# Kernel tuning notes

Measured on AMD Instinct MI355X. Metric: run time of the kernel, lower is better.

The kernel has to match this reference:

```python
import jax, jax.numpy as jnp
import numpy as np

N, D, L = 8192, 256, 3
DEGREE_P = 0.0078  # ~64 avg degree


def _normalize_adj(g):
    # symmetric normalization with self-loops: D^-1/2 (A + I) D^-1/2
    n = g.shape[0]
    a = g + jnp.eye(n, dtype=g.dtype)
    deg = jnp.sum(a, axis=1)
    dinv = jnp.where(deg > 0, jax.lax.rsqrt(deg), 0.0)
    return a * dinv[:, None] * dinv[None, :]


def _gcn(gn, h, W, b):
    # GCN layer (eval mode, dropout p=0): aggregate -> linear -> relu
    h = gn @ h                      # [N, D] adjacency aggregation
    return jax.nn.relu(h @ W.T + b)  # [N, D]


def setup_inputs() -> dict:
    key = jax.random.key(0)
    ks = jax.random.split(key, 8)
    # sparse binary symmetric adjacency stored dense
    g = (jax.random.uniform(ks[0], (N, N)) < DEGREE_P).astype(jnp.float32)
    g = jnp.maximum(g, g.T)
    h = jax.random.normal(ks[1], (N, D), dtype=jnp.float32)
    s = 1.0 / np.sqrt(D)
    W_down = jax.random.normal(ks[2], (L, D, D), dtype=jnp.float32) * s
    b_down = jnp.zeros((L, D), dtype=jnp.float32)
    W_bottom = jax.random.normal(ks[3], (D, D), dtype=jnp.float32) * s
    b_bottom = jnp.zeros((D,), dtype=jnp.float32)
    W_up = jax.random.normal(ks[4], (L, D, D), dtype=jnp.float32) * s
    b_up = jnp.zeros((L, D), dtype=jnp.float32)
    return dict(g=g, h=h, W_down=W_down, b_down=b_down,
                W_bottom=W_bottom, b_bottom=b_bottom,
                W_up=W_up, b_up=b_up)


def reference(g, h, W_down, b_down, W_bottom, b_bottom, W_up, b_up):
    gn = _normalize_adj(g)
    l_n = W_down.shape[0]
    org_h = h
    down_outs = []
    for i in range(l_n):
        h = _gcn(gn, h, W_down[i], b_down[i])
        down_outs.append(h)
    h = _gcn(gn, h, W_bottom, b_bottom)
    hs = []
    for i in range(l_n):
        h = h + down_outs[l_n - i - 1]   # skip connection
        h = _gcn(gn, h, W_up[i], b_up[i])
        hs.append(h)
    hs.append(h + org_h)
    return jnp.stack(hs)  # [l_n+1, N, D]
```

## Files before the change

### kernel.cpp

```cpp
#include <hip/hip_runtime.h>
#include <cstdint>
#include <cstddef>


#define GN 8192
#define GD 256
#define CAP 320

typedef unsigned int uint32;
using frag_ab = __attribute__((ext_vector_type(8))) short;
using frag_cd = __attribute__((ext_vector_type(4))) float;
using f32x4   = __attribute__((ext_vector_type(4))) float;
using u32x2   = __attribute__((ext_vector_type(2))) uint32;

static __device__ inline unsigned short f2bf(float x) {
    uint32 u = __float_as_uint(x);
    u += 0x7fffu + ((u >> 16) & 1u);
    return (unsigned short)(u >> 16);
}

__global__ __launch_bounds__(256) void k_build(const float* __restrict__ g,
                                               unsigned short* __restrict__ col,
                                               int* __restrict__ cnt,
                                               float* __restrict__ dinv)
{
    __shared__ int s_cnt;
    const int i = blockIdx.x;
    const int tid = threadIdx.x;
    if (tid == 0) s_cnt = 0;
    __syncthreads();
    const f32x4* grow = (const f32x4*)(g + (size_t)i * GN);
    unsigned short* crow = col + (size_t)i * CAP;
    for (int j4 = tid; j4 < GN / 4; j4 += 256) {
        f32x4 v = __builtin_nontemporal_load(grow + j4);
        int j = j4 * 4;
        if (v[0] != 0.0f) { int p = atomicAdd(&s_cnt, 1); if (p < CAP) __builtin_nontemporal_store((unsigned short)(j + 0), crow + p); }
        if (v[1] != 0.0f) { int p = atomicAdd(&s_cnt, 1); if (p < CAP) __builtin_nontemporal_store((unsigned short)(j + 1), crow + p); }
        if (v[2] != 0.0f) { int p = atomicAdd(&s_cnt, 1); if (p < CAP) __builtin_nontemporal_store((unsigned short)(j + 2), crow + p); }
        if (v[3] != 0.0f) { int p = atomicAdd(&s_cnt, 1); if (p < CAP) __builtin_nontemporal_store((unsigned short)(j + 3), crow + p); }
    }
    __syncthreads();
    if (tid == 0) {
        int n = s_cnt; if (n > CAP) n = CAP;
        cnt[i] = n;
        dinv[i] = rsqrtf((float)s_cnt + 1.0f);
    }
}

__global__ __launch_bounds__(256) void k_scale(const float* __restrict__ h,
                                               const float* __restrict__ dinv,
                                               unsigned short* __restrict__ hs_bf)
{
    int idx = blockIdx.x * 256 + threadIdx.x;
    float4 v = ((const float4*)h)[idx];
    int row = idx / (GD / 4);
    float dv = dinv[row];
    ushort4 r;
    r.x = f2bf(v.x * dv); r.y = f2bf(v.y * dv);
    r.z = f2bf(v.z * dv); r.w = f2bf(v.w * dv);
    ((ushort4*)hs_bf)[idx] = r;
}

__global__ __launch_bounds__(256) void k_f2bf(const float* __restrict__ src,
                                              unsigned short* __restrict__ dst)
{
    int idx = blockIdx.x * 256 + threadIdx.x;
    float4 v = ((const float4*)src)[idx];
    ushort4 r;
    r.x = f2bf(v.x); r.y = f2bf(v.y); r.z = f2bf(v.z); r.w = f2bf(v.w);
    ((ushort4*)dst)[idx] = r;
}

__global__ __launch_bounds__(256) void k_spmm(const u32x2* __restrict__ hsw,
                                              const unsigned short* __restrict__ col,
                                              const int* __restrict__ cnt,
                                              const float* __restrict__ dinv,
                                              u32x2* __restrict__ yw)
{
    __shared__ unsigned short s_cols[4][CAP];
    const int tid  = threadIdx.x;
    const int lr   = tid >> 6;
    const int lane = tid & 63;
    const int i    = blockIdx.x * 4 + lr;
    const int n    = cnt[i];
    unsigned short* sc = s_cols[lr];
    const unsigned short* crow = col + (size_t)i * CAP;
    for (int t = lane; t < n; t += 64)
        sc[t] = __builtin_nontemporal_load(crow + t);

    float e0a = 0.f, e1a = 0.f, e2a = 0.f, e3a = 0.f;
    float e0b = 0.f, e1b = 0.f, e2b = 0.f, e3b = 0.f;
    int t = 0;
    for (; t + 8 <= n; t += 8) {
        ushort4 ca = *(const ushort4*)(sc + t);
        ushort4 cb = *(const ushort4*)(sc + t + 4);
        u32x2 u0 = hsw[(uint32)ca.x * 64u + lane];
        u32x2 u1 = hsw[(uint32)ca.y * 64u + lane];
        u32x2 u2 = hsw[(uint32)ca.z * 64u + lane];
        u32x2 u3 = hsw[(uint32)ca.w * 64u + lane];
        u32x2 u4 = hsw[(uint32)cb.x * 64u + lane];
        u32x2 u5 = hsw[(uint32)cb.y * 64u + lane];
        u32x2 u6 = hsw[(uint32)cb.z * 64u + lane];
        u32x2 u7 = hsw[(uint32)cb.w * 64u + lane];
        e0a += __uint_as_float(u0[0] << 16); e1a += __uint_as_float(u0[0] & 0xffff0000u);
        e2a += __uint_as_float(u0[1] << 16); e3a += __uint_as_float(u0[1] & 0xffff0000u);
        e0b += __uint_as_float(u1[0] << 16); e1b += __uint_as_float(u1[0] & 0xffff0000u);
        e2b += __uint_as_float(u1[1] << 16); e3b += __uint_as_float(u1[1] & 0xffff0000u);
        e0a += __uint_as_float(u2[0] << 16); e1a += __uint_as_float(u2[0] & 0xffff0000u);
        e2a += __uint_as_float(u2[1] << 16); e3a += __uint_as_float(u2[1] & 0xffff0000u);
        e0b += __uint_as_float(u3[0] << 16); e1b += __uint_as_float(u3[0] & 0xffff0000u);
        e2b += __uint_as_float(u3[1] << 16); e3b += __uint_as_float(u3[1] & 0xffff0000u);
        e0a += __uint_as_float(u4[0] << 16); e1a += __uint_as_float(u4[0] & 0xffff0000u);
        e2a += __uint_as_float(u4[1] << 16); e3a += __uint_as_float(u4[1] & 0xffff0000u);
        e0b += __uint_as_float(u5[0] << 16); e1b += __uint_as_float(u5[0] & 0xffff0000u);
        e2b += __uint_as_float(u5[1] << 16); e3b += __uint_as_float(u5[1] & 0xffff0000u);
        e0a += __uint_as_float(u6[0] << 16); e1a += __uint_as_float(u6[0] & 0xffff0000u);
        e2a += __uint_as_float(u6[1] << 16); e3a += __uint_as_float(u6[1] & 0xffff0000u);
        e0b += __uint_as_float(u7[0] << 16); e1b += __uint_as_float(u7[0] & 0xffff0000u);
        e2b += __uint_as_float(u7[1] << 16); e3b += __uint_as_float(u7[1] & 0xffff0000u);
    }
    for (; t < n; ++t) {
        u32x2 u = hsw[(uint32)sc[t] * 64u + lane];
        e0a += __uint_as_float(u[0] << 16); e1a += __uint_as_float(u[0] & 0xffff0000u);
        e2a += __uint_as_float(u[1] << 16); e3a += __uint_as_float(u[1] & 0xffff0000u);
    }
    u32x2 us = hsw[(uint32)i * 64u + lane];
    e0b += __uint_as_float(us[0] << 16); e1b += __uint_as_float(us[0] & 0xffff0000u);
    e2b += __uint_as_float(us[1] << 16); e3b += __uint_as_float(us[1] & 0xffff0000u);

    const float dv = dinv[i];
    const float e0 = (e0a + e0b) * dv;
    const float e1 = (e1a + e1b) * dv;
    const float e2 = (e2a + e2b) * dv;
    const float e3 = (e3a + e3b) * dv;
    u32x2 r;
    r[0] = (uint32)f2bf(e0) | ((uint32)f2bf(e1) << 16);
    r[1] = (uint32)f2bf(e2) | ((uint32)f2bf(e3) << 16);
    __builtin_nontemporal_store(r, yw + (uint32)i * 64u + lane);
}

__global__ __launch_bounds__(256) void k_gemm(const unsigned short* __restrict__ Y,
                                              const unsigned short* __restrict__ W,
                                              const float* __restrict__ bias,
                                              const float* __restrict__ dinv,
                                              const float* __restrict__ skip,
                                              float* __restrict__ h_out,
                                              unsigned short* __restrict__ hs_out,
                                              float* __restrict__ sum_out,
                                              const float* __restrict__ add_src)
{
    const int tid  = threadIdx.x;
    const int w    = tid >> 6;
    const int lane = tid & 63;
    const int quad = lane >> 4;
    const int l16  = lane & 15;
    const int m0 = blockIdx.x * 64 + w * 16;
    const int n0 = blockIdx.y * 64;

    frag_cd acc0 = {0.f,0.f,0.f,0.f}, acc1 = {0.f,0.f,0.f,0.f};
    frag_cd acc2 = {0.f,0.f,0.f,0.f}, acc3 = {0.f,0.f,0.f,0.f};

    const size_t abase  = (size_t)(m0 + l16) * GD + quad * 8;
    const size_t bbase0 = (size_t)(n0 +  0 + l16) * GD + quad * 8;
    const size_t bbase1 = (size_t)(n0 + 16 + l16) * GD + quad * 8;
    const size_t bbase2 = (size_t)(n0 + 32 + l16) * GD + quad * 8;
    const size_t bbase3 = (size_t)(n0 + 48 + l16) * GD + quad * 8;

#pragma unroll
    for (int k0 = 0; k0 < GD; k0 += 32) {
        frag_ab a  = *(const frag_ab*)(Y + abase  + k0);
        frag_ab b0 = *(const frag_ab*)(W + bbase0 + k0);
        frag_ab b1 = *(const frag_ab*)(W + bbase1 + k0);
        frag_ab b2 = *(const frag_ab*)(W + bbase2 + k0);
        frag_ab b3 = *(const frag_ab*)(W + bbase3 + k0);
        acc0 = __builtin_amdgcn_mfma_f32_16x16x32_bf16(a, b0, acc0, 0, 0, 0);
        acc1 = __builtin_amdgcn_mfma_f32_16x16x32_bf16(a, b1, acc1, 0, 0, 0);
        acc2 = __builtin_amdgcn_mfma_f32_16x16x32_bf16(a, b2, acc2, 0, 0, 0);
        acc3 = __builtin_amdgcn_mfma_f32_16x16x32_bf16(a, b3, acc3, 0, 0, 0);
    }

    const float bn0 = bias[n0 +  0 + l16];
    const float bn1 = bias[n0 + 16 + l16];
    const float bn2 = bias[n0 + 32 + l16];
    const float bn3 = bias[n0 + 48 + l16];

#pragma unroll
    for (int reg = 0; reg < 4; ++reg) {
        const int m = m0 + quad * 4 + reg;
        const float dv = dinv[m];
        float v[4];
        v[0] = fmaxf(acc0[reg] + bn0, 0.f);
        v[1] = fmaxf(acc1[reg] + bn1, 0.f);
        v[2] = fmaxf(acc2[reg] + bn2, 0.f);
        v[3] = fmaxf(acc3[reg] + bn3, 0.f);
#pragma unroll
        for (int nt = 0; nt < 4; ++nt) {
            const size_t idx = (size_t)m * GD + n0 + nt * 16 + l16;
            const float x = v[nt];
            if (h_out)  __builtin_nontemporal_store(x, h_out + idx);
            if (hs_out) {
                float s = skip ? __builtin_nontemporal_load(skip + idx) : 0.f;
                hs_out[idx] = f2bf(dv * (x + s));
            }
            if (sum_out) __builtin_nontemporal_store(x + __builtin_nontemporal_load(add_src + idx), sum_out + idx);
        }
    }
}

extern "C" void kernel_launch(void* const* d_in, const int* in_sizes, int n_in,
                              void* d_out, int out_size, void* d_ws, size_t ws_size,
                              hipStream_t stream)
{
    const float* g  = (const float*)d_in[0];
    const float* h  = (const float*)d_in[1];
    const float* Wd = (const float*)d_in[2];
    const float* bd = (const float*)d_in[3];
    const float* Wb = (const float*)d_in[4];
    const float* bb = (const float*)d_in[5];
    const float* Wu = (const float*)d_in[6];
    const float* bu = (const float*)d_in[7];
    float* out = (float*)d_out;

    char* ws = (char*)d_ws;
    float*          dinv = (float*)ws;
    int*            cnt  = (int*)(ws + 32 * 1024);
    unsigned short* col  = (unsigned short*)(ws + 64 * 1024);
    size_t off = 64 * 1024 + (size_t)GN * CAP * sizeof(unsigned short);
    off = (off + 255) & ~(size_t)255;
    unsigned short* hs_bf = (unsigned short*)(ws + off); off += (size_t)GN * GD * 2;
    unsigned short* y_bf  = (unsigned short*)(ws + off); off += (size_t)GN * GD * 2;
    unsigned short* w_bf  = (unsigned short*)(ws + off); off += (size_t)7 * GD * GD * 2;
    off = (off + 255) & ~(size_t)255;
    float* dbuf1 = (float*)(ws + off); off += (size_t)GN * GD * 4;
    float* dbuf2 = (float*)(ws + off); off += (size_t)GN * GD * 4;
    float* dbuf3 = (float*)(ws + off); off += (size_t)GN * GD * 4;
    (void)ws_size; (void)in_sizes; (void)n_in; (void)out_size;

    const size_t ND = (size_t)GN * GD;
    const int WSZ = GD * GD;
    dim3 ggrid(GN / 64, GD / 64);

    k_build<<<GN, 256, 0, stream>>>(g, col, cnt, dinv);
    k_scale<<<GN * GD / 4 / 256, 256, 0, stream>>>(h, dinv, hs_bf);
    k_f2bf<<<3 * WSZ / 4 / 256, 256, 0, stream>>>(Wd, w_bf + 0 * (size_t)WSZ);
    k_f2bf<<<1 * WSZ / 4 / 256, 256, 0, stream>>>(Wb, w_bf + 3 * (size_t)WSZ);
    k_f2bf<<<3 * WSZ / 4 / 256, 256, 0, stream>>>(Wu, w_bf + 4 * (size_t)WSZ);

    k_spmm<<<GN / 4, 256, 0, stream>>>((const u32x2*)hs_bf, col, cnt, dinv, (u32x2*)y_bf);
    k_gemm<<<ggrid, 256, 0, stream>>>(y_bf, w_bf + 0 * (size_t)WSZ, bd + 0 * GD, dinv, nullptr, dbuf1, hs_bf, nullptr, nullptr);
    k_spmm<<<GN / 4, 256, 0, stream>>>((const u32x2*)hs_bf, col, cnt, dinv, (u32x2*)y_bf);
    k_gemm<<<ggrid, 256, 0, stream>>>(y_bf, w_bf + 1 * (size_t)WSZ, bd + 1 * GD, dinv, nullptr, dbuf2, hs_bf, nullptr, nullptr);
    k_spmm<<<GN / 4, 256, 0, stream>>>((const u32x2*)hs_bf, col, cnt, dinv, (u32x2*)y_bf);
    k_gemm<<<ggrid, 256, 0, stream>>>(y_bf, w_bf + 2 * (size_t)WSZ, bd + 2 * GD, dinv, nullptr, dbuf3, hs_bf, nullptr, nullptr);

    k_spmm<<<GN / 4, 256, 0, stream>>>((const u32x2*)hs_bf, col, cnt, dinv, (u32x2*)y_bf);
    k_gemm<<<ggrid, 256, 0, stream>>>(y_bf, w_bf + 3 * (size_t)WSZ, bb, dinv, dbuf3, nullptr, hs_bf, nullptr, nullptr);

    k_spmm<<<GN / 4, 256, 0, stream>>>((const u32x2*)hs_bf, col, cnt, dinv, (u32x2*)y_bf);
    k_gemm<<<ggrid, 256, 0, stream>>>(y_bf, w_bf + 4 * (size_t)WSZ, bu + 0 * GD, dinv, dbuf2, out + 0 * ND, hs_bf, nullptr, nullptr);
    k_spmm<<<GN / 4, 256, 0, stream>>>((const u32x2*)hs_bf, col, cnt, dinv, (u32x2*)y_bf);
    k_gemm<<<ggrid, 256, 0, stream>>>(y_bf, w_bf + 5 * (size_t)WSZ, bu + 1 * GD, dinv, dbuf1, out + 1 * ND, hs_bf, nullptr, nullptr);
    k_spmm<<<GN / 4, 256, 0, stream>>>((const u32x2*)hs_bf, col, cnt, dinv, (u32x2*)y_bf);
    k_gemm<<<ggrid, 256, 0, stream>>>(y_bf, w_bf + 6 * (size_t)WSZ, bu + 2 * GD, dinv, nullptr, out + 2 * ND, nullptr, out + 3 * ND, h);
}
```

Measured before the change: 763.6 us.

## Fuse sparse aggregation and dense GEMM into one per-layer kernel via LDS

Each GCN layer now runs as one kernel: a block gathers neighbor rows for 16 nodes, writes the aggregated bf16 tile into swizzled shared memory, then runs MFMA against W with the existing epilogue. This drops the global round trip of the intermediate Y buffer and halves the kernel launches. The h-scaling and weight conversion kernels are merged into one prep launch, and ping-pong hs buffers replace the in-place update. Nontemporal load/store hints are also removed. Each block now covers only 16 rows and all 256 output columns, so W is reloaded per 16 rows and the gather phase has fewer independent waves to overlap latency.

```diff
diff --git a/kernel.cpp b/kernel.cpp
--- a/kernel.cpp
+++ b/kernel.cpp
@@ -10,7 +10,6 @@
 typedef unsigned int uint32;
 using frag_ab = __attribute__((ext_vector_type(8))) short;
 using frag_cd = __attribute__((ext_vector_type(4))) float;
-using f32x4   = __attribute__((ext_vector_type(4))) float;
 using u32x2   = __attribute__((ext_vector_type(2))) uint32;
 
 static __device__ inline unsigned short f2bf(float x) {
@@ -29,15 +28,15 @@
     const int tid = threadIdx.x;
     if (tid == 0) s_cnt = 0;
     __syncthreads();
-    const f32x4* grow = (const f32x4*)(g + (size_t)i * GN);
+    const float4* grow = (const float4*)(g + (size_t)i * GN);
     unsigned short* crow = col + (size_t)i * CAP;
     for (int j4 = tid; j4 < GN / 4; j4 += 256) {
-        f32x4 v = __builtin_nontemporal_load(grow + j4);
+        float4 v = grow[j4];
         int j = j4 * 4;
-        if (v[0] != 0.0f) { int p = atomicAdd(&s_cnt, 1); if (p < CAP) __builtin_nontemporal_store((unsigned short)(j + 0), crow + p); }
-        if (v[1] != 0.0f) { int p = atomicAdd(&s_cnt, 1); if (p < CAP) __builtin_nontemporal_store((unsigned short)(j + 1), crow + p); }
-        if (v[2] != 0.0f) { int p = atomicAdd(&s_cnt, 1); if (p < CAP) __builtin_nontemporal_store((unsigned short)(j + 2), crow + p); }
-        if (v[3] != 0.0f) { int p = atomicAdd(&s_cnt, 1); if (p < CAP) __builtin_nontemporal_store((unsigned short)(j + 3), crow + p); }
+        if (v.x != 0.0f) { int p = atomicAdd(&s_cnt, 1); if (p < CAP) crow[p] = (unsigned short)(j + 0); }
+        if (v.y != 0.0f) { int p = atomicAdd(&s_cnt, 1); if (p < CAP) crow[p] = (unsigned short)(j + 1); }
+        if (v.z != 0.0f) { int p = atomicAdd(&s_cnt, 1); if (p < CAP) crow[p] = (unsigned short)(j + 2); }
+        if (v.w != 0.0f) { int p = atomicAdd(&s_cnt, 1); if (p < CAP) crow[p] = (unsigned short)(j + 3); }
     }
     __syncthreads();
     if (tid == 0) {
@@ -47,132 +46,141 @@
     }
 }
 
-__global__ __launch_bounds__(256) void k_scale(const float* __restrict__ h,
-                                               const float* __restrict__ dinv,
-                                               unsigned short* __restrict__ hs_bf)
-{
-    int idx = blockIdx.x * 256 + threadIdx.x;
-    float4 v = ((const float4*)h)[idx];
-    int row = idx / (GD / 4);
-    float dv = dinv[row];
-    ushort4 r;
-    r.x = f2bf(v.x * dv); r.y = f2bf(v.y * dv);
-    r.z = f2bf(v.z * dv); r.w = f2bf(v.w * dv);
-    ((ushort4*)hs_bf)[idx] = r;
-}
-
-__global__ __launch_bounds__(256) void k_f2bf(const float* __restrict__ src,
-                                              unsigned short* __restrict__ dst)
-{
-    int idx = blockIdx.x * 256 + threadIdx.x;
-    float4 v = ((const float4*)src)[idx];
+__global__ __launch_bounds__(256) void k_prep(const float* __restrict__ h,
+                                              const float* __restrict__ dinv,
+                                              unsigned short* __restrict__ hs,
+                                              const float* __restrict__ Wd,
+                                              const float* __restrict__ Wb,
+                                              const float* __restrict__ Wu,
+                                              unsigned short* __restrict__ w_bf)
+{
+    const int WSZ = GD * GD;
+    int bid = blockIdx.x;
+    if (bid < 2048) {
+        int idx = bid * 256 + threadIdx.x;
+        float4 v = ((const float4*)h)[idx];
+        int row = idx >> 6;
+        float dv = dinv[row];
+        ushort4 r;
+        r.x = f2bf(v.x * dv); r.y = f2bf(v.y * dv);
+        r.z = f2bf(v.z * dv); r.w = f2bf(v.w * dv);
+        ((ushort4*)hs)[idx] = r;
+        return;
+    }
+    bid -= 2048;
+    const float* src;
+    unsigned short* dst;
+    if (bid < 192)      { src = Wd + (size_t)bid * 1024;        dst = w_bf + (size_t)bid * 1024; }
+    else if (bid < 256) { src = Wb + (size_t)(bid - 192) * 1024; dst = w_bf + 3 * (size_t)WSZ + (size_t)(bid - 192) * 1024; }
+    else                { src = Wu + (size_t)(bid - 256) * 1024; dst = w_bf + 4 * (size_t)WSZ + (size_t)(bid - 256) * 1024; }
+    int t = threadIdx.x;
+    float4 v = ((const float4*)src)[t];
     ushort4 r;
     r.x = f2bf(v.x); r.y = f2bf(v.y); r.z = f2bf(v.z); r.w = f2bf(v.w);
-    ((ushort4*)dst)[idx] = r;
-}
-
-__global__ __launch_bounds__(256) void k_spmm(const u32x2* __restrict__ hsw,
-                                              const unsigned short* __restrict__ col,
-                                              const int* __restrict__ cnt,
-                                              const float* __restrict__ dinv,
-                                              u32x2* __restrict__ yw)
+    ((ushort4*)dst)[t] = r;
+}
+
+__global__ __launch_bounds__(256) void k_layer(const u32x2* __restrict__ hsw,
+                                               const unsigned short* __restrict__ col,
+                                               const int* __restrict__ cnt,
+                                               const float* __restrict__ dinv,
+                                               const unsigned short* __restrict__ W,
+                                               const float* __restrict__ bias,
+                                               const float* __restrict__ skip,
+                                               float* __restrict__ h_out,
+                                               unsigned short* __restrict__ hs_out,
+                                               float* __restrict__ sum_out,
+                                               const float* __restrict__ add_src)
 {
     __shared__ unsigned short s_cols[4][CAP];
-    const int tid  = threadIdx.x;
-    const int lr   = tid >> 6;
-    const int lane = tid & 63;
-    const int i    = blockIdx.x * 4 + lr;
-    const int n    = cnt[i];
-    unsigned short* sc = s_cols[lr];
-    const unsigned short* crow = col + (size_t)i * CAP;
-    for (int t = lane; t < n; t += 64)
-        sc[t] = __builtin_nontemporal_load(crow + t);
-
-    float e0a = 0.f, e1a = 0.f, e2a = 0.f, e3a = 0.f;
-    float e0b = 0.f, e1b = 0.f, e2b = 0.f, e3b = 0.f;
-    int t = 0;
-    for (; t + 8 <= n; t += 8) {
-        ushort4 ca = *(const ushort4*)(sc + t);
-        ushort4 cb = *(const ushort4*)(sc + t + 4);
-        u32x2 u0 = hsw[(uint32)ca.x * 64u + lane];
-        u32x2 u1 = hsw[(uint32)ca.y * 64u + lane];
-        u32x2 u2 = hsw[(uint32)ca.z * 64u + lane];
-        u32x2 u3 = hsw[(uint32)ca.w * 64u + lane];
-        u32x2 u4 = hsw[(uint32)cb.x * 64u + lane];
-        u32x2 u5 = hsw[(uint32)cb.y * 64u + lane];
-        u32x2 u6 = hsw[(uint32)cb.z * 64u + lane];
-        u32x2 u7 = hsw[(uint32)cb.w * 64u + lane];
-        e0a += __uint_as_float(u0[0] << 16); e1a += __uint_as_float(u0[0] & 0xffff0000u);
-        e2a += __uint_as_float(u0[1] << 16); e3a += __uint_as_float(u0[1] & 0xffff0000u);
-        e0b += __uint_as_float(u1[0] << 16); e1b += __uint_as_float(u1[0] & 0xffff0000u);
-        e2b += __uint_as_float(u1[1] << 16); e3b += __uint_as_float(u1[1] & 0xffff0000u);
-        e0a += __uint_as_float(u2[0] << 16); e1a += __uint_as_float(u2[0] & 0xffff0000u);
-        e2a += __uint_as_float(u2[1] << 16); e3a += __uint_as_float(u2[1] & 0xffff0000u);
-        e0b += __uint_as_float(u3[0] << 16); e1b += __uint_as_float(u3[0] & 0xffff0000u);
-        e2b += __uint_as_float(u3[1] << 16); e3b += __uint_as_float(u3[1] & 0xffff0000u);
-        e0a += __uint_as_float(u4[0] << 16); e1a += __uint_as_float(u4[0] & 0xffff0000u);
-        e2a += __uint_as_float(u4[1] << 16); e3a += __uint_as_float(u4[1] & 0xffff0000u);
-        e0b += __uint_as_float(u5[0] << 16); e1b += __uint_as_float(u5[0] & 0xffff0000u);
-        e2b += __uint_as_float(u5[1] << 16); e3b += __uint_as_float(u5[1] & 0xffff0000u);
-        e0a += __uint_as_float(u6[0] << 16); e1a += __uint_as_float(u6[0] & 0xffff0000u);
-        e2a += __uint_as_float(u6[1] << 16); e3a += __uint_as_float(u6[1] & 0xffff0000u);
-        e0b += __uint_as_float(u7[0] << 16); e1b += __uint_as_float(u7[0] & 0xffff0000u);
-        e2b += __uint_as_float(u7[1] << 16); e3b += __uint_as_float(u7[1] & 0xffff0000u);
-    }
-    for (; t < n; ++t) {
-        u32x2 u = hsw[(uint32)sc[t] * 64u + lane];
-        e0a += __uint_as_float(u[0] << 16); e1a += __uint_as_float(u[0] & 0xffff0000u);
-        e2a += __uint_as_float(u[1] << 16); e3a += __uint_as_float(u[1] & 0xffff0000u);
-    }
-    u32x2 us = hsw[(uint32)i * 64u + lane];
-    e0b += __uint_as_float(us[0] << 16); e1b += __uint_as_float(us[0] & 0xffff0000u);
-    e2b += __uint_as_float(us[1] << 16); e3b += __uint_as_float(us[1] & 0xffff0000u);
-
-    const float dv = dinv[i];
-    const float e0 = (e0a + e0b) * dv;
-    const float e1 = (e1a + e1b) * dv;
-    const float e2 = (e2a + e2b) * dv;
-    const float e3 = (e3a + e3b) * dv;
-    u32x2 r;
-    r[0] = (uint32)f2bf(e0) | ((uint32)f2bf(e1) << 16);
-    r[1] = (uint32)f2bf(e2) | ((uint32)f2bf(e3) << 16);
-    __builtin_nontemporal_store(r, yw + (uint32)i * 64u + lane);
-}
-
-__global__ __launch_bounds__(256) void k_gemm(const unsigned short* __restrict__ Y,
-                                              const unsigned short* __restrict__ W,
-                                              const float* __restrict__ bias,
-                                              const float* __restrict__ dinv,
-                                              const float* __restrict__ skip,
-                                              float* __restrict__ h_out,
-                                              unsigned short* __restrict__ hs_out,
-                                              float* __restrict__ sum_out,
-                                              const float* __restrict__ add_src)
-{
+    __shared__ unsigned short s_y[16 * GD];
+
     const int tid  = threadIdx.x;
     const int w    = tid >> 6;
     const int lane = tid & 63;
     const int quad = lane >> 4;
     const int l16  = lane & 15;
-    const int m0 = blockIdx.x * 64 + w * 16;
-    const int n0 = blockIdx.y * 64;
-
+    const int rbase = blockIdx.x * 16;
+
+    unsigned short* sc = s_cols[w];
+    for (int rr = 0; rr < 4; ++rr) {
+        const int r = w * 4 + rr;
+        const int i = rbase + r;
+        const int n = cnt[i];
+        const unsigned short* crow = col + (size_t)i * CAP;
+        for (int t = lane; t < n; t += 64) sc[t] = crow[t];
+
+        float e0a = 0.f, e1a = 0.f, e2a = 0.f, e3a = 0.f;
+        float e0b = 0.f, e1b = 0.f, e2b = 0.f, e3b = 0.f;
+        int t = 0;
+        for (; t + 8 <= n; t += 8) {
+            ushort4 ca = *(const ushort4*)(sc + t);
+            ushort4 cb = *(const ushort4*)(sc + t + 4);
+            u32x2 u0 = hsw[(uint32)ca.x * 64u + lane];
+            u32x2 u1 = hsw[(uint32)ca.y * 64u + lane];
+            u32x2 u2 = hsw[(uint32)ca.z * 64u + lane];
+            u32x2 u3 = hsw[(uint32)ca.w * 64u + lane];
+            u32x2 u4 = hsw[(uint32)cb.x * 64u + lane];
+            u32x2 u5 = hsw[(uint32)cb.y * 64u + lane];
+            u32x2 u6 = hsw[(uint32)cb.z * 64u + lane];
+            u32x2 u7 = hsw[(uint32)cb.w * 64u + lane];
+            e0a += __uint_as_float(u0[0] << 16); e1a += __uint_as_float(u0[0] & 0xffff0000u);
+            e2a += __uint_as_float(u0[1] << 16); e3a += __uint_as_float(u0[1] & 0xffff0000u);
+            e0b += __uint_as_float(u1[0] << 16); e1b += __uint_as_float(u1[0] & 0xffff0000u);
+            e2b += __uint_as_float(u1[1] << 16); e3b += __uint_as_float(u1[1] & 0xffff0000u);
+            e0a += __uint_as_float(u2[0] << 16); e1a += __uint_as_float(u2[0] & 0xffff0000u);
+            e2a += __uint_as_float(u2[1] << 16); e3a += __uint_as_float(u2[1] & 0xffff0000u);
+            e0b += __uint_as_float(u3[0] << 16); e1b += __uint_as_float(u3[0] & 0xffff0000u);
+            e2b += __uint_as_float(u3[1] << 16); e3b += __uint_as_float(u3[1] & 0xffff0000u);
+            e0a += __uint_as_float(u4[0] << 16); e1a += __uint_as_float(u4[0] & 0xffff0000u);
+            e2a += __uint_as_float(u4[1] << 16); e3a += __uint_as_float(u4[1] & 0xffff0000u);
+            e0b += __uint_as_float(u5[0] << 16); e1b += __uint_as_float(u5[0] & 0xffff0000u);
+            e2b += __uint_as_float(u5[1] << 16); e3b += __uint_as_float(u5[1] & 0xffff0000u);
+            e0a += __uint_as_float(u6[0] << 16); e1a += __uint_as_float(u6[0] & 0xffff0000u);
+            e2a += __uint_as_float(u6[1] << 16); e3a += __uint_as_float(u6[1] & 0xffff0000u);
+            e0b += __uint_as_float(u7[0] << 16); e1b += __uint_as_float(u7[0] & 0xffff0000u);
+            e2b += __uint_as_float(u7[1] << 16); e3b += __uint_as_float(u7[1] & 0xffff0000u);
+        }
+        for (; t < n; ++t) {
+            u32x2 u = hsw[(uint32)sc[t] * 64u + lane];
+            e0a += __uint_as_float(u[0] << 16); e1a += __uint_as_float(u[0] & 0xffff0000u);
+            e2a += __uint_as_float(u[1] << 16); e3a += __uint_as_float(u[1] & 0xffff0000u);
+        }
+        u32x2 us = hsw[(uint32)i * 64u + lane];
+        e0b += __uint_as_float(us[0] << 16); e1b += __uint_as_float(us[0] & 0xffff0000u);
+        e2b += __uint_as_float(us[1] << 16); e3b += __uint_as_float(us[1] & 0xffff0000u);
+
+        const float dv = dinv[i];
+        const float e0 = (e0a + e0b) * dv;
+        const float e1 = (e1a + e1b) * dv;
+        const float e2 = (e2a + e2b) * dv;
+        const float e3 = (e3a + e3b) * dv;
+        u32x2 rv;
+        rv[0] = (uint32)f2bf(e0) | ((uint32)f2bf(e1) << 16);
+        rv[1] = (uint32)f2bf(e2) | ((uint32)f2bf(e3) << 16);
+        const uint32 ba = (uint32)r * 512u + (uint32)lane * 8u;
+        *(u32x2*)((char*)s_y + (ba ^ ((uint32)(r & 7) << 4))) = rv;
+    }
+    __syncthreads();
+
+    const int n0 = w * 64;
     frag_cd acc0 = {0.f,0.f,0.f,0.f}, acc1 = {0.f,0.f,0.f,0.f};
     frag_cd acc2 = {0.f,0.f,0.f,0.f}, acc3 = {0.f,0.f,0.f,0.f};
 
-    const size_t abase  = (size_t)(m0 + l16) * GD + quad * 8;
-    const size_t bbase0 = (size_t)(n0 +  0 + l16) * GD + quad * 8;
-    const size_t bbase1 = (size_t)(n0 + 16 + l16) * GD + quad * 8;
-    const size_t bbase2 = (size_t)(n0 + 32 + l16) * GD + quad * 8;
-    const size_t bbase3 = (size_t)(n0 + 48 + l16) * GD + quad * 8;
+    const uint32 aoff = (uint32)l16 * 512u + (uint32)quad * 16u;
+    const uint32 aX   = ((uint32)(l16 & 7)) << 4;
+    const size_t bb0 = (size_t)(n0 +  0 + l16) * GD + quad * 8;
+    const size_t bb1 = (size_t)(n0 + 16 + l16) * GD + quad * 8;
+    const size_t bb2 = (size_t)(n0 + 32 + l16) * GD + quad * 8;
+    const size_t bb3 = (size_t)(n0 + 48 + l16) * GD + quad * 8;
 
 #pragma unroll
     for (int k0 = 0; k0 < GD; k0 += 32) {
-        frag_ab a  = *(const frag_ab*)(Y + abase  + k0);
-        frag_ab b0 = *(const frag_ab*)(W + bbase0 + k0);
-        frag_ab b1 = *(const frag_ab*)(W + bbase1 + k0);
-        frag_ab b2 = *(const frag_ab*)(W + bbase2 + k0);
-        frag_ab b3 = *(const frag_ab*)(W + bbase3 + k0);
+        frag_ab a  = *(const frag_ab*)((const char*)s_y + ((aoff + (uint32)k0 * 2u) ^ aX));
+        frag_ab b0 = *(const frag_ab*)(W + bb0 + k0);
+        frag_ab b1 = *(const frag_ab*)(W + bb1 + k0);
+        frag_ab b2 = *(const frag_ab*)(W + bb2 + k0);
+        frag_ab b3 = *(const frag_ab*)(W + bb3 + k0);
         acc0 = __builtin_amdgcn_mfma_f32_16x16x32_bf16(a, b0, acc0, 0, 0, 0);
         acc1 = __builtin_amdgcn_mfma_f32_16x16x32_bf16(a, b1, acc1, 0, 0, 0);
         acc2 = __builtin_amdgcn_mfma_f32_16x16x32_bf16(a, b2, acc2, 0, 0, 0);
@@ -186,8 +194,8 @@
 
 #pragma unroll
     for (int reg = 0; reg < 4; ++reg) {
-        const int m = m0 + quad * 4 + reg;
-        const float dv = dinv[m];
+        const int m = rbase + quad * 4 + reg;
+        const float dvm = dinv[m];
         float v[4];
         v[0] = fmaxf(acc0[reg] + bn0, 0.f);
         v[1] = fmaxf(acc1[reg] + bn1, 0.f);
@@ -197,12 +205,12 @@
         for (int nt = 0; nt < 4; ++nt) {
             const size_t idx = (size_t)m * GD + n0 + nt * 16 + l16;
             const float x = v[nt];
-            if (h_out)  __builtin_nontemporal_store(x, h_out + idx);
+            if (h_out)  h_out[idx] = x;
             if (hs_out) {
-                float s = skip ? __builtin_nontemporal_load(skip + idx) : 0.f;
-                hs_out[idx] = f2bf(dv * (x + s));
+                float s = skip ? skip[idx] : 0.f;
+                hs_out[idx] = f2bf(dvm * (x + s));
             }
-            if (sum_out) __builtin_nontemporal_store(x + __builtin_nontemporal_load(add_src + idx), sum_out + idx);
+            if (sum_out) sum_out[idx] = x + add_src[idx];
         }
     }
 }
@@ -227,9 +235,9 @@
     unsigned short* col  = (unsigned short*)(ws + 64 * 1024);
     size_t off = 64 * 1024 + (size_t)GN * CAP * sizeof(unsigned short);
     off = (off + 255) & ~(size_t)255;
-    unsigned short* hs_bf = (unsigned short*)(ws + off); off += (size_t)GN * GD * 2;
-    unsigned short* y_bf  = (unsigned short*)(ws + off); off += (size_t)GN * GD * 2;
-    unsigned short* w_bf  = (unsigned short*)(ws + off); off += (size_t)7 * GD * GD * 2;
+    unsigned short* hs0 = (unsigned short*)(ws + off); off += (size_t)GN * GD * 2;
+    unsigned short* hs1 = (unsigned short*)(ws + off); off += (size_t)GN * GD * 2;
+    unsigned short* w_bf = (unsigned short*)(ws + off); off += (size_t)7 * GD * GD * 2;
     off = (off + 255) & ~(size_t)255;
     float* dbuf1 = (float*)(ws + off); off += (size_t)GN * GD * 4;
     float* dbuf2 = (float*)(ws + off); off += (size_t)GN * GD * 4;
@@ -238,28 +246,24 @@
 
     const size_t ND = (size_t)GN * GD;
     const int WSZ = GD * GD;
-    dim3 ggrid(GN / 64, GD / 64);
 
     k_build<<<GN, 256, 0, stream>>>(g, col, cnt, dinv);
-    k_scale<<<GN * GD / 4 / 256, 256, 0, stream>>>(h, dinv, hs_bf);
-    k_f2bf<<<3 * WSZ / 4 / 256, 256, 0, stream>>>(Wd, w_bf + 0 * (size_t)WSZ);
-    k_f2bf<<<1 * WSZ / 4 / 256, 256, 0, stream>>>(Wb, w_bf + 3 * (size_t)WSZ);
-    k_f2bf<<<3 * WSZ / 4 / 256, 256, 0, stream>>>(Wu, w_bf + 4 * (size_t)WSZ);
-
-    k_spmm<<<GN / 4, 256, 0, stream>>>((const u32x2*)hs_bf, col, cnt, dinv, (u32x2*)y_bf);
-    k_gemm<<<ggrid, 256, 0, stream>>>(y_bf, w_bf + 0 * (size_t)WSZ, bd + 0 * GD, dinv, nullptr, dbuf1, hs_bf, nullptr, nullptr);
-    k_spmm<<<GN / 4, 256, 0, stream>>>((const u32x2*)hs_bf, col, cnt, dinv, (u32x2*)y_bf);
-    k_gemm<<<ggrid, 256, 0, stream>>>(y_bf, w_bf + 1 * (size_t)WSZ, bd + 1 * GD, dinv, nullptr, dbuf2, hs_bf, nullptr, nullptr);
-    k_spmm<<<GN / 4, 256, 0, stream>>>((const u32x2*)hs_bf, col, cnt, dinv, (u32x2*)y_bf);
-    k_gemm<<<ggrid, 256, 0, stream>>>(y_bf, w_bf + 2 * (size_t)WSZ, bd + 2 * GD, dinv, nullptr, dbuf3, hs_bf, nullptr, nullptr);
-
-    k_spmm<<<GN / 4, 256, 0, stream>>>((const u32x2*)hs_bf, col, cnt, dinv, (u32x2*)y_bf);
-    k_gemm<<<ggrid, 256, 0, stream>>>(y_bf, w_bf + 3 * (size_t)WSZ, bb, dinv, dbuf3, nullptr, hs_bf, nullptr, nullptr);
-
-    k_spmm<<<GN / 4, 256, 0, stream>>>((const u32x2*)hs_bf, col, cnt, dinv, (u32x2*)y_bf);
-    k_gemm<<<ggrid, 256, 0, stream>>>(y_bf, w_bf + 4 * (size_t)WSZ, bu + 0 * GD, dinv, dbuf2, out + 0 * ND, hs_bf, nullptr, nullptr);
-    k_spmm<<<GN / 4, 256, 0, stream>>>((const u32x2*)hs_bf, col, cnt, dinv, (u32x2*)y_bf);
-    k_gemm<<<ggrid, 256, 0, stream>>>(y_bf, w_bf + 5 * (size_t)WSZ, bu + 1 * GD, dinv, dbuf1, out + 1 * ND, hs_bf, nullptr, nullptr);
-    k_spmm<<<GN / 4, 256, 0, stream>>>((const u32x2*)hs_bf, col, cnt, dinv, (u32x2*)y_bf);
-    k_gemm<<<ggrid, 256, 0, stream>>>(y_bf, w_bf + 6 * (size_t)WSZ, bu + 2 * GD, dinv, nullptr, out + 2 * ND, nullptr, out + 3 * ND, h);
-}
+    k_prep<<<2496, 256, 0, stream>>>(h, dinv, hs0, Wd, Wb, Wu, w_bf);
+
+    k_layer<<<GN / 16, 256, 0, stream>>>((const u32x2*)hs0, col, cnt, dinv,
+        w_bf + 0 * (size_t)WSZ, bd + 0 * GD, nullptr, dbuf1, hs1, nullptr, nullptr);
+    k_layer<<<GN / 16, 256, 0, stream>>>((const u32x2*)hs1, col, cnt, dinv,
+        w_bf + 1 * (size_t)WSZ, bd + 1 * GD, nullptr, dbuf2, hs0, nullptr, nullptr);
+    k_layer<<<GN / 16, 256, 0, stream>>>((const u32x2*)hs0, col, cnt, dinv,
+        w_bf + 2 * (size_t)WSZ, bd + 2 * GD, nullptr, dbuf3, hs1, nullptr, nullptr);
+
+    k_layer<<<GN / 16, 256, 0, stream>>>((const u32x2*)hs1, col, cnt, dinv,
+        w_bf + 3 * (size_t)WSZ, bb, dbuf3, nullptr, hs0, nullptr, nullptr);
+
+    k_layer<<<GN / 16, 256, 0, stream>>>((const u32x2*)hs0, col, cnt, dinv,
+        w_bf + 4 * (size_t)WSZ, bu + 0 * GD, dbuf2, out + 0 * ND, hs1, nullptr, nullptr);
+    k_layer<<<GN / 16, 256, 0, stream>>>((const u32x2*)hs1, col, cnt, dinv,
+        w_bf + 5 * (size_t)WSZ, bu + 1 * GD, dbuf1, out + 1 * ND, hs0, nullptr, nullptr);
+    k_layer<<<GN / 16, 256, 0, stream>>>((const u32x2*)hs0, col, cnt, dinv,
+        w_bf + 6 * (size_t)WSZ, bu + 2 * GD, nullptr, out + 2 * ND, nullptr, out + 3 * ND, h);
+}
```

Measured after the change: 759.6 us. No clear change (-0.5%).
